# Kernel tuning notes

Measured on AMD Instinct MI355X. Metric: run time of the kernel, lower is better.

## Reference

```python
import jax, jax.numpy as jnp
import numpy as np

T, B, E, H = 2048, 2, 1024, 16

def setup_inputs() -> dict:
    rng = jax.random.key(0)
    ks = jax.random.split(rng, 7)
    s = 0.02
    return {
        "query": jax.random.normal(ks[0], (T, B, E), jnp.float32),
        "key": jax.random.normal(ks[1], (T, B, E), jnp.float32),
        "value": jax.random.normal(ks[2], (T, B, E), jnp.float32),
        "in_proj_weight": jax.random.normal(ks[3], (3 * E, E), jnp.float32) * s,
        "in_proj_bias": jax.random.normal(ks[4], (3 * E,), jnp.float32) * s,
        "out_proj_weight": jax.random.normal(ks[5], (E, E), jnp.float32) * s,
        "out_proj_bias": jax.random.normal(ks[6], (E,), jnp.float32) * s,
    }

def reference(query, key, value, in_proj_weight, in_proj_bias, out_proj_weight, out_proj_bias):
    tgt_len, bsz, embed_dim = query.shape
    num_heads = H
    head_dim = embed_dim // num_heads
    scaling = head_dim ** -0.5
    wq, wk, wv = jnp.split(in_proj_weight, 3, axis=0)
    bq, bk, bv = jnp.split(in_proj_bias, 3, axis=0)
    # projections: F.linear(x, W, b) = x @ W.T + b
    q = (query @ wq.T + bq) * scaling          # (T, B, E)
    k = key @ wk.T + bk                        # (S, B, E)
    v = value @ wv.T + bv                      # (S, B, E)
    # (len, B, E) -> (B*H, len, head_dim), matching torch view+transpose
    def to_heads(x):
        L = x.shape[0]
        return x.reshape(L, bsz * num_heads, head_dim).transpose(1, 0, 2)
    q, k, v = to_heads(q), to_heads(k), to_heads(v)
    scores = jnp.einsum('bqd,bkd->bqk', q, k)  # (B*H, T, S)
    attn = jax.nn.softmax(scores, axis=-1)
    out = jnp.einsum('bqk,bkd->bqd', attn, v)  # (B*H, T, head_dim)
    out = out.transpose(1, 0, 2).reshape(tgt_len, bsz, embed_dim)
    out = out @ out_proj_weight.T + out_proj_bias
    return out
```

## Files before the change

### kernel.cpp

```cpp
#include <hip/hip_runtime.h>
#include <cstdint>
#include <cstddef>

#define QSCALE 0.18033688011112042f

typedef __attribute__((ext_vector_type(8))) short bf16x8;
typedef __attribute__((ext_vector_type(4))) float f32x4;

#define MFMA(a, b, c) __builtin_amdgcn_mfma_f32_16x16x32_bf16(a, b, c, 0, 0, 0)

typedef union { unsigned int u[4]; bf16x8 b; } pku;

__device__ __forceinline__ unsigned short cvt_bf16(float x) {
  union { float f; unsigned int u; } v;
  v.f = x;
  unsigned int r = v.u + 0x7FFFu + ((v.u >> 16) & 1u);
  return (unsigned short)(r >> 16);
}

__device__ __forceinline__ void gll16(const void* g, void* l) {
  __builtin_amdgcn_global_load_lds(
      (const __attribute__((address_space(1))) unsigned int*)g,
      (__attribute__((address_space(3))) unsigned int*)l, 16, 0, 0);
}

__device__ __forceinline__ float fast_exp2(float x) {
#if __has_builtin(__builtin_amdgcn_exp2f)
  return __builtin_amdgcn_exp2f(x);
#else
  float r; asm("v_exp_f32 %0, %1" : "=v"(r) : "v"(x)); return r;
#endif
}

__device__ __forceinline__ unsigned int pack_bf16(float lo, float hi) {
  union { float f; unsigned int u; } a, b;
  a.f = lo; b.f = hi;
  return __builtin_amdgcn_perm(b.u + 0x8000u, a.u + 0x8000u, 0x07060302u);
}

__global__ void cvt_all(const float* __restrict__ q,
                        const float* __restrict__ k,
                        const float* __restrict__ v,
                        const float* __restrict__ ipw,
                        const float* __restrict__ opw,
                        unsigned short* __restrict__ dst) {
  const size_t i = ((size_t)blockIdx.x * 256 + threadIdx.x) * 8;
  const float* src;
  float scale = 1.0f;
  if (i < 4194304) src = q + i;
  else if (i < 8388608) src = k + (i - 4194304);
  else if (i < 12582912) src = v + (i - 8388608);
  else {
    const size_t w = i - 12582912;
    if (w < 3145728) { src = ipw + w; if (w < 1048576) scale = QSCALE; }
    else src = opw + (w - 3145728);
  }
  float4 a = *(const float4*)src;
  float4 b = *(const float4*)(src + 4);
  uint4 o;
  o.x = cvt_bf16(a.x * scale) | ((unsigned int)cvt_bf16(a.y * scale) << 16);
  o.y = cvt_bf16(a.z * scale) | ((unsigned int)cvt_bf16(a.w * scale) << 16);
  o.z = cvt_bf16(b.x * scale) | ((unsigned int)cvt_bf16(b.y * scale) << 16);
  o.w = cvt_bf16(b.z * scale) | ((unsigned int)cvt_bf16(b.w * scale) << 16);
  *(uint4*)(dst + i) = o;
}

__global__ __launch_bounds__(256, 3) void gemm_qkv(
    const unsigned short* __restrict__ X,
    const unsigned short* __restrict__ W,
    const float* __restrict__ bias,
    unsigned short* __restrict__ Qh,
    unsigned short* __restrict__ Kh,
    unsigned short* __restrict__ Vt)
{
  __shared__ unsigned short As[128 * 64];
  __shared__ unsigned short Bs[128 * 64];
  const int tid = threadIdx.x;
  const int wave = tid >> 6, lane = tid & 63;
  const int quad = lane >> 4, l16 = lane & 15;
  const int flat = blockIdx.x + (blockIdx.y << 3) + (blockIdx.z << 8);
  const int nf = (flat & 7) * 96 + (flat >> 3);
  const int z = nf >> 8;
  const int m0 = ((nf >> 3) & 31) * 128;
  const int n0 = (nf & 7) * 128;
  const unsigned short* Ab = X + (size_t)z * 4194304 + (size_t)m0 * 1024;
  const unsigned short* Bb = W + ((size_t)z * 1024 + n0) * 1024;
  const int wr = (wave >> 1) * 64, wc = (wave & 1) * 64;

  const f32x4 z4 = {0.f, 0.f, 0.f, 0.f};
  f32x4 acc[4][4];
#pragma unroll
  for (int i = 0; i < 4; ++i)
#pragma unroll
    for (int j = 0; j < 4; ++j) acc[i][j] = z4;

  for (int k0 = 0; k0 < 1024; k0 += 64) {
    __syncthreads();
#pragma unroll
    for (int j = 0; j < 4; ++j) {
      const int c = j * 256 + tid;
      const int row = c >> 3, pc = c & 7;
      const int kc = pc ^ (row & 7);
      gll16(Ab + (size_t)row * 1024 + k0 + kc * 8, &As[c * 8]);
      gll16(Bb + (size_t)row * 1024 + k0 + kc * 8, &Bs[c * 8]);
    }
    __syncthreads();
#pragma unroll
    for (int kk = 0; kk < 2; ++kk) {
      bf16x8 af[4], bfr[4];
#pragma unroll
      for (int rt = 0; rt < 4; ++rt) {
        const int row = wr + rt * 16 + l16;
        af[rt] = *(const bf16x8*)&As[row * 64 + ((kk * 4 + quad) ^ (row & 7)) * 8];
      }
#pragma unroll
      for (int ct = 0; ct < 4; ++ct) {
        const int row = wc + ct * 16 + l16;
        bfr[ct] = *(const bf16x8*)&Bs[row * 64 + ((kk * 4 + quad) ^ (row & 7)) * 8];
      }
#pragma unroll
      for (int rt = 0; rt < 4; ++rt)
#pragma unroll
        for (int ct = 0; ct < 4; ++ct)
          acc[rt][ct] = MFMA(af[rt], bfr[ct], acc[rt][ct]);
    }
  }

#pragma unroll
  for (int rt = 0; rt < 4; ++rt)
#pragma unroll
    for (int ct = 0; ct < 4; ++ct) {
      const int gn = n0 + wc + ct * 16 + l16;
      float bv = bias[z * 1024 + gn];
      if (z == 0) bv *= QSCALE;
      const int h = gn >> 6, d = gn & 63;
#pragma unroll
      for (int r = 0; r < 4; ++r) {
        const int gm = m0 + wr + rt * 16 + quad * 4 + r;
        const int t = gm >> 1, b = gm & 1;
        const int bh = b * 16 + h;
        const unsigned short o = cvt_bf16(acc[rt][ct][r] + bv);
        if (z == 0)      Qh[((size_t)bh * 2048 + t) * 64 + d] = o;
        else if (z == 1) Kh[((size_t)bh * 2048 + t) * 64 + d] = o;
        else {
          const int w32 = t & 31;
          const int tp = (t & ~31) | (((w32 >> 2) & 3) << 3) | ((w32 >> 4) << 2) | (w32 & 3);
          Vt[((size_t)bh * 64 + d) * 2048 + tp] = o;
        }
      }
    }
}

__global__ __launch_bounds__(256, 2) void attn(
    const unsigned short* __restrict__ Qh,
    const unsigned short* __restrict__ Kh,
    const unsigned short* __restrict__ Vt,
    unsigned short* __restrict__ O)
{
  __shared__ unsigned short KV[2][16384];
  __shared__ float Ls[128];
  const int tid = threadIdx.x;
  const int wave = tid >> 6, lane = tid & 63;
  const int quad = lane >> 4, l16 = lane & 15;
  const int pair = wave >> 1, kh = wave & 1;
  const int flat = blockIdx.x + (blockIdx.y << 4);
  const int nf = (flat & 7) * 64 + (flat >> 3);
  const int qt = nf & 15, bh = nf >> 4;
  const unsigned short* Qb = Qh + ((size_t)bh * 2048 + qt * 128 + pair * 64) * 64;
  const unsigned short* Kb = Kh + (size_t)bh * 2048 * 64;
  const unsigned short* Vb = Vt + (size_t)bh * 64 * 2048;

  bf16x8 qf[4][2];
#pragma unroll
  for (int g = 0; g < 4; ++g)
#pragma unroll
    for (int kk = 0; kk < 2; ++kk)
      qf[g][kk] = *(const bf16x8*)(Qb + (size_t)(g * 16 + l16) * 64 + kk * 32 + quad * 8);

  const unsigned short* kp[4];
  const unsigned short* vp[4];
  int klo[4], vlo[4];
#pragma unroll
  for (int j = 0; j < 4; ++j) {
    const int c = wave * 256 + j * 64 + lane;
    const int r = c >> 3, cc = c & 7;
    kp[j] = Kb + (size_t)r * 64 + (cc ^ (r & 7)) * 8;
    klo[j] = c * 8;
    const int r2 = c >> 4, cc2 = c & 15;
    vp[j] = Vb + (size_t)r2 * 2048 + (cc2 ^ (r2 & 15)) * 8;
    vlo[j] = 8192 + c * 8;
  }

  pku ones;
  ones.u[0] = ones.u[1] = ones.u[2] = ones.u[3] = 0x3F803F80u;

  const f32x4 z4 = {0.f, 0.f, 0.f, 0.f};
  f32x4 oacc[4][4];
  f32x4 lacc[4] = {z4, z4, z4, z4};
#pragma unroll
  for (int g = 0; g < 4; ++g)
#pragma unroll
    for (int c = 0; c < 4; ++c) oacc[g][c] = z4;

#pragma unroll
  for (int j = 0; j < 4; ++j) {
    gll16(kp[j], &KV[0][klo[j]]);
    gll16(vp[j], &KV[0][vlo[j]]);
    kp[j] += 128 * 64;
    vp[j] += 128;
  }
  __syncthreads();

#pragma unroll 1
  for (int it = 0; it < 16; ++it) {
    const int cur = it & 1;
    if (it < 15) {
#pragma unroll
      for (int j = 0; j < 4; ++j) {
        gll16(kp[j], &KV[cur ^ 1][klo[j]]);
        gll16(vp[j], &KV[cur ^ 1][vlo[j]]);
        kp[j] += 128 * 64;
        vp[j] += 128;
      }
    }
    const unsigned short* Ks = KV[cur];
    const unsigned short* Vs = KV[cur] + 8192;

#pragma unroll
    for (int jj = 0; jj < 2; ++jj) {
      unsigned int pk0[4][2], pk1[4][2];
#pragma unroll
      for (int half = 0; half < 2; ++half) {
        const int ct = jj * 2 + half;
        const int R = kh * 64 + ct * 16 + l16;
        bf16x8 kfr[2];
#pragma unroll
        for (int kk = 0; kk < 2; ++kk)
          kfr[kk] = *(const bf16x8*)&Ks[R * 64 + ((kk * 4 + quad) ^ (R & 7)) * 8];
#pragma unroll
        for (int g = 0; g < 4; ++g) {
          f32x4 sv = z4;
          sv = MFMA(kfr[0], qf[g][0], sv);
          sv = MFMA(kfr[1], qf[g][1], sv);
          f32x4 p;
#pragma unroll
          for (int r = 0; r < 4; ++r) p[r] = fast_exp2(sv[r]);
          pk0[g][half] = pack_bf16(p[0], p[1]);
          pk1[g][half] = pack_bf16(p[2], p[3]);
        }
      }
      const int jjg = kh * 2 + jj;
#pragma unroll
      for (int ctd = 0; ctd < 4; ++ctd) {
        const int R = ctd * 16 + l16;
        const int phys = (jjg * 4 + quad) ^ (R & 15);
        const bf16x8 vv = *(const bf16x8*)&Vs[R * 128 + phys * 8];
#pragma unroll
        for (int g = 0; g < 4; ++g) {
          pku a;
          a.u[0] = pk0[g][0]; a.u[1] = pk1[g][0];
          a.u[2] = pk0[g][1]; a.u[3] = pk1[g][1];
          oacc[g][ctd] = MFMA(a.b, vv, oacc[g][ctd]);
        }
      }
#pragma unroll
      for (int g = 0; g < 4; ++g) {
        pku a;
        a.u[0] = pk0[g][0]; a.u[1] = pk1[g][0];
        a.u[2] = pk0[g][1]; a.u[3] = pk1[g][1];
        lacc[g] = MFMA(a.b, ones.b, lacc[g]);
      }
    }
    __syncthreads();
  }

  float* Fp = (float*)KV;
  if (kh == 1) {
#pragma unroll
    for (int g = 0; g < 4; ++g) {
#pragma unroll
      for (int ctd = 0; ctd < 4; ++ctd)
#pragma unroll
        for (int r = 0; r < 4; ++r)
          Fp[pair * 4096 + (g * 16 + quad * 4 + r) * 64 + ctd * 16 + l16] = oacc[g][ctd][r];
#pragma unroll
      for (int r = 0; r < 4; ++r)
        Ls[pair * 64 + g * 16 + quad * 4 + r] = lacc[g][r];
    }
  }
  __syncthreads();
  if (kh == 0) {
    const int b = bh >> 4, h = bh & 15;
#pragma unroll
    for (int g = 0; g < 4; ++g)
#pragma unroll
      for (int r = 0; r < 4; ++r) {
        const int ql = g * 16 + quad * 4 + r;
        const float lv = lacc[g][r] + Ls[pair * 64 + ql];
        const float inv = 1.0f / lv;
        const int t = qt * 128 + pair * 64 + ql;
#pragma unroll
        for (int ctd = 0; ctd < 4; ++ctd) {
          const float val = oacc[g][ctd][r] + Fp[pair * 4096 + ql * 64 + ctd * 16 + l16];
          O[((size_t)t * 2 + b) * 1024 + h * 64 + ctd * 16 + l16] = cvt_bf16(val * inv);
        }
      }
  }
}

__global__ __launch_bounds__(256, 2) void gemm_out(
    const unsigned short* __restrict__ A,
    const unsigned short* __restrict__ W,
    const float* __restrict__ bias,
    float* __restrict__ out)
{
  __shared__ unsigned short As[2][128 * 64];
  __shared__ unsigned short Bs[2][64 * 64];
  const int tid = threadIdx.x;
  const int wave = tid >> 6, lane = tid & 63;
  const int quad = lane >> 4, l16 = lane & 15;
  const int flat = blockIdx.x + (blockIdx.y << 4);
  const int nf = (flat & 7) * 64 + (flat >> 3);
  const int m0 = (nf >> 4) * 128;
  const int n0 = (nf & 15) * 64;
  const unsigned short* Ab = A + (size_t)m0 * 1024;
  const unsigned short* Bb = W + (size_t)n0 * 1024;
  const int wr = (wave >> 1) * 64, wc = (wave & 1) * 32;

  auto stage = [&](int k0, int buf) {
#pragma unroll
    for (int j = 0; j < 4; ++j) {
      const int c = j * 256 + tid;
      const int row = c >> 3, pc = c & 7;
      const int kc = pc ^ (row & 7);
      gll16(Ab + (size_t)row * 1024 + k0 + kc * 8, &As[buf][c * 8]);
    }
#pragma unroll
    for (int j = 0; j < 2; ++j) {
      const int c = j * 256 + tid;
      const int row = c >> 3, pc = c & 7;
      const int kc = pc ^ (row & 7);
      gll16(Bb + (size_t)row * 1024 + k0 + kc * 8, &Bs[buf][c * 8]);
    }
  };

  const f32x4 z4 = {0.f, 0.f, 0.f, 0.f};
  f32x4 acc[4][2];
#pragma unroll
  for (int i = 0; i < 4; ++i)
#pragma unroll
    for (int j = 0; j < 2; ++j) acc[i][j] = z4;

  stage(0, 0);
  __syncthreads();

  for (int k0 = 0; k0 < 1024; k0 += 64) {
    const int cur = (k0 >> 6) & 1;
    if (k0 < 960) stage(k0 + 64, cur ^ 1);
#pragma unroll
    for (int kk = 0; kk < 2; ++kk) {
      bf16x8 af[4], bfr[2];
#pragma unroll
      for (int rt = 0; rt < 4; ++rt) {
        const int row = wr + rt * 16 + l16;
        af[rt] = *(const bf16x8*)&As[cur][row * 64 + ((kk * 4 + quad) ^ (row & 7)) * 8];
      }
#pragma unroll
      for (int ct = 0; ct < 2; ++ct) {
        const int row = wc + ct * 16 + l16;
        bfr[ct] = *(const bf16x8*)&Bs[cur][row * 64 + ((kk * 4 + quad) ^ (row & 7)) * 8];
      }
#pragma unroll
      for (int rt = 0; rt < 4; ++rt)
#pragma unroll
        for (int ct = 0; ct < 2; ++ct)
          acc[rt][ct] = MFMA(af[rt], bfr[ct], acc[rt][ct]);
    }
    __syncthreads();
  }

#pragma unroll
  for (int rt = 0; rt < 4; ++rt)
#pragma unroll
    for (int ct = 0; ct < 2; ++ct) {
      const int gn = n0 + wc + ct * 16 + l16;
      const float bv = bias[gn];
#pragma unroll
      for (int r = 0; r < 4; ++r) {
        const int gm = m0 + wr + rt * 16 + quad * 4 + r;
        out[(size_t)gm * 1024 + gn] = acc[rt][ct][r] + bv;
      }
    }
}

extern "C" void kernel_launch(void* const* d_in, const int* in_sizes, int n_in,
                              void* d_out, int out_size, void* d_ws, size_t ws_size,
                              hipStream_t stream) {
  const float* q   = (const float*)d_in[0];
  const float* k   = (const float*)d_in[1];
  const float* v   = (const float*)d_in[2];
  const float* ipw = (const float*)d_in[3];
  const float* ipb = (const float*)d_in[4];
  const float* opw = (const float*)d_in[5];
  const float* opb = (const float*)d_in[6];

  unsigned short* ws = (unsigned short*)d_ws;
  unsigned short* X  = ws;
  unsigned short* Wb = ws + 12582912;
  unsigned short* Wo = ws + 15728640;
  unsigned short* Qh = ws + 16777216;
  unsigned short* Kh = ws + 20971520;
  unsigned short* Vx = ws + 25165824;
  unsigned short* Oa = ws + 29360128;

  cvt_all<<<dim3(8192), 256, 0, stream>>>(q, k, v, ipw, opw, ws);
  gemm_qkv<<<dim3(8, 32, 3), 256, 0, stream>>>(X, Wb, ipb, Qh, Kh, Vx);
  attn<<<dim3(16, 32), 256, 0, stream>>>(Qh, Kh, Vx, Oa);
  gemm_out<<<dim3(16, 32), 256, 0, stream>>>(Oa, Wo, opb, (float*)d_out);
}
```

Before: 211.2 us.

## Double-buffer QKV GEMM and use single explicit waitcnt barrier per pipeline step

The QKV projection GEMM moves from a single shared buffer with two barriers per k-step to a double-buffered pipeline, prefetching the next k-tile while the current one runs on MFMA. Its occupancy hint drops from 3 to 2 blocks per CU to make room for the larger shared buffer. All three kernels (QKV GEMM, attention, out-proj GEMM) replace their end-of-iteration __syncthreads with one PIPE_SYNC at the top of each step: an explicit vmcnt(0) wait plus s_barrier fenced by sched_barriers. The goal is to overlap global-to-LDS loads with compute and cut barrier count, at the cost of lower occupancy in the QKV GEMM.

```diff
diff --git a/kernel.cpp b/kernel.cpp
--- a/kernel.cpp
+++ b/kernel.cpp
@@ -8,6 +8,13 @@
 typedef __attribute__((ext_vector_type(4))) float f32x4;
 
 #define MFMA(a, b, c) __builtin_amdgcn_mfma_f32_16x16x32_bf16(a, b, c, 0, 0, 0)
+
+#define PIPE_SYNC() do {                                   \
+    asm volatile("s_waitcnt vmcnt(0)" ::: "memory");       \
+    __builtin_amdgcn_sched_barrier(0);                     \
+    __builtin_amdgcn_s_barrier();                          \
+    __builtin_amdgcn_sched_barrier(0);                     \
+  } while (0)
 
 typedef union { unsigned int u[4]; bf16x8 b; } pku;
 
@@ -65,7 +72,7 @@
   *(uint4*)(dst + i) = o;
 }
 
-__global__ __launch_bounds__(256, 3) void gemm_qkv(
+__global__ __launch_bounds__(256, 2) void gemm_qkv(
     const unsigned short* __restrict__ X,
     const unsigned short* __restrict__ W,
     const float* __restrict__ bias,
@@ -73,8 +80,7 @@
     unsigned short* __restrict__ Kh,
     unsigned short* __restrict__ Vt)
 {
-  __shared__ unsigned short As[128 * 64];
-  __shared__ unsigned short Bs[128 * 64];
+  __shared__ unsigned short S[2][16384];
   const int tid = threadIdx.x;
   const int wave = tid >> 6, lane = tid & 63;
   const int quad = lane >> 4, l16 = lane & 15;
@@ -94,17 +100,26 @@
 #pragma unroll
     for (int j = 0; j < 4; ++j) acc[i][j] = z4;
 
-  for (int k0 = 0; k0 < 1024; k0 += 64) {
-    __syncthreads();
+  auto stage = [&](int k0, int buf) {
 #pragma unroll
     for (int j = 0; j < 4; ++j) {
       const int c = j * 256 + tid;
       const int row = c >> 3, pc = c & 7;
       const int kc = pc ^ (row & 7);
-      gll16(Ab + (size_t)row * 1024 + k0 + kc * 8, &As[c * 8]);
-      gll16(Bb + (size_t)row * 1024 + k0 + kc * 8, &Bs[c * 8]);
-    }
-    __syncthreads();
+      gll16(Ab + (size_t)row * 1024 + k0 + kc * 8, &S[buf][c * 8]);
+      gll16(Bb + (size_t)row * 1024 + k0 + kc * 8, &S[buf][8192 + c * 8]);
+    }
+  };
+
+  stage(0, 0);
+
+#pragma unroll 1
+  for (int t = 0; t < 16; ++t) {
+    const int cur = t & 1;
+    PIPE_SYNC();
+    if (t < 15) stage((t + 1) * 64, cur ^ 1);
+    const unsigned short* As = S[cur];
+    const unsigned short* Bs = S[cur] + 8192;
 #pragma unroll
     for (int kk = 0; kk < 2; ++kk) {
       bf16x8 af[4], bfr[4];
@@ -209,11 +224,11 @@
     kp[j] += 128 * 64;
     vp[j] += 128;
   }
-  __syncthreads();
 
 #pragma unroll 1
   for (int it = 0; it < 16; ++it) {
     const int cur = it & 1;
+    PIPE_SYNC();
     if (it < 15) {
 #pragma unroll
       for (int j = 0; j < 4; ++j) {
@@ -271,9 +286,9 @@
         lacc[g] = MFMA(a.b, ones.b, lacc[g]);
       }
     }
-    __syncthreads();
-  }
-
+  }
+
+  __syncthreads();
   float* Fp = (float*)KV;
   if (kh == 1) {
 #pragma unroll
@@ -352,10 +367,11 @@
     for (int j = 0; j < 2; ++j) acc[i][j] = z4;
 
   stage(0, 0);
-  __syncthreads();
-
+
+#pragma unroll 1
   for (int k0 = 0; k0 < 1024; k0 += 64) {
     const int cur = (k0 >> 6) & 1;
+    PIPE_SYNC();
     if (k0 < 960) stage(k0 + 64, cur ^ 1);
 #pragma unroll
     for (int kk = 0; kk < 2; ++kk) {
@@ -376,7 +392,6 @@
         for (int ct = 0; ct < 2; ++ct)
           acc[rt][ct] = MFMA(af[rt], bfr[ct], acc[rt][ct]);
     }
-    __syncthreads();
   }
 
 #pragma unroll
```

Result: no change. 211.4 us (+0.1%).

## Fuse fp32-to-bf16 conversion into GEMM loads and tighten attention pipeline sync

Applied to the files above, without the earlier changes.

Drops the separate conversion kernel. The QKV and output GEMMs now read fp32 inputs and weights directly and convert to bf16 while writing to LDS, which removes one launch and a full bf16 round trip through global memory. The attention loop moves its barrier to the top of each iteration with an explicit vmcnt wait and raises wave priority around the PV MFMAs. The cost is that the GEMMs lose async global-to-LDS loads: gemm_out drops to single buffering with higher occupancy, and each GEMM block re-converts the weights it reads instead of using a precomputed bf16 copy.

```diff
diff --git a/kernel.cpp b/kernel.cpp
--- a/kernel.cpp
+++ b/kernel.cpp
@@ -8,6 +8,13 @@
 typedef __attribute__((ext_vector_type(4))) float f32x4;
 
 #define MFMA(a, b, c) __builtin_amdgcn_mfma_f32_16x16x32_bf16(a, b, c, 0, 0, 0)
+
+#define PIPE_SYNC() do {                                   \
+    asm volatile("s_waitcnt vmcnt(0)" ::: "memory");       \
+    __builtin_amdgcn_sched_barrier(0);                     \
+    __builtin_amdgcn_s_barrier();                          \
+    __builtin_amdgcn_sched_barrier(0);                     \
+  } while (0)
 
 typedef union { unsigned int u[4]; bf16x8 b; } pku;
 
@@ -38,36 +45,20 @@
   return __builtin_amdgcn_perm(b.u + 0x8000u, a.u + 0x8000u, 0x07060302u);
 }
 
-__global__ void cvt_all(const float* __restrict__ q,
-                        const float* __restrict__ k,
-                        const float* __restrict__ v,
-                        const float* __restrict__ ipw,
-                        const float* __restrict__ opw,
-                        unsigned short* __restrict__ dst) {
-  const size_t i = ((size_t)blockIdx.x * 256 + threadIdx.x) * 8;
-  const float* src;
-  float scale = 1.0f;
-  if (i < 4194304) src = q + i;
-  else if (i < 8388608) src = k + (i - 4194304);
-  else if (i < 12582912) src = v + (i - 8388608);
-  else {
-    const size_t w = i - 12582912;
-    if (w < 3145728) { src = ipw + w; if (w < 1048576) scale = QSCALE; }
-    else src = opw + (w - 3145728);
-  }
-  float4 a = *(const float4*)src;
-  float4 b = *(const float4*)(src + 4);
+__device__ __forceinline__ uint4 cvt8(float4 a, float4 b, float sc) {
   uint4 o;
-  o.x = cvt_bf16(a.x * scale) | ((unsigned int)cvt_bf16(a.y * scale) << 16);
-  o.y = cvt_bf16(a.z * scale) | ((unsigned int)cvt_bf16(a.w * scale) << 16);
-  o.z = cvt_bf16(b.x * scale) | ((unsigned int)cvt_bf16(b.y * scale) << 16);
-  o.w = cvt_bf16(b.z * scale) | ((unsigned int)cvt_bf16(b.w * scale) << 16);
-  *(uint4*)(dst + i) = o;
+  o.x = pack_bf16(a.x * sc, a.y * sc);
+  o.y = pack_bf16(a.z * sc, a.w * sc);
+  o.z = pack_bf16(b.x * sc, b.y * sc);
+  o.w = pack_bf16(b.z * sc, b.w * sc);
+  return o;
 }
 
 __global__ __launch_bounds__(256, 3) void gemm_qkv(
-    const unsigned short* __restrict__ X,
-    const unsigned short* __restrict__ W,
+    const float* __restrict__ Qf,
+    const float* __restrict__ Kf,
+    const float* __restrict__ Vf,
+    const float* __restrict__ Wf,
     const float* __restrict__ bias,
     unsigned short* __restrict__ Qh,
     unsigned short* __restrict__ Kh,
@@ -83,8 +74,9 @@
   const int z = nf >> 8;
   const int m0 = ((nf >> 3) & 31) * 128;
   const int n0 = (nf & 7) * 128;
-  const unsigned short* Ab = X + (size_t)z * 4194304 + (size_t)m0 * 1024;
-  const unsigned short* Bb = W + ((size_t)z * 1024 + n0) * 1024;
+  const float* Ab = (z == 0 ? Qf : (z == 1 ? Kf : Vf)) + (size_t)m0 * 1024;
+  const float* Bb = Wf + ((size_t)z * 1024 + n0) * 1024;
+  const float wsc = (z == 0) ? QSCALE : 1.0f;
   const int wr = (wave >> 1) * 64, wc = (wave & 1) * 64;
 
   const f32x4 z4 = {0.f, 0.f, 0.f, 0.f};
@@ -100,9 +92,15 @@
     for (int j = 0; j < 4; ++j) {
       const int c = j * 256 + tid;
       const int row = c >> 3, pc = c & 7;
-      const int kc = pc ^ (row & 7);
-      gll16(Ab + (size_t)row * 1024 + k0 + kc * 8, &As[c * 8]);
-      gll16(Bb + (size_t)row * 1024 + k0 + kc * 8, &Bs[c * 8]);
+      const int swz = (pc ^ (row & 7)) * 8;
+      const float* sa = Ab + (size_t)row * 1024 + k0 + pc * 8;
+      const float4 a0 = *(const float4*)sa;
+      const float4 a1 = *(const float4*)(sa + 4);
+      *(uint4*)&As[row * 64 + swz] = cvt8(a0, a1, 1.0f);
+      const float* sb = Bb + (size_t)row * 1024 + k0 + pc * 8;
+      const float4 b0 = *(const float4*)sb;
+      const float4 b1 = *(const float4*)(sb + 4);
+      *(uint4*)&Bs[row * 64 + swz] = cvt8(b0, b1, wsc);
     }
     __syncthreads();
 #pragma unroll
@@ -209,11 +207,11 @@
     kp[j] += 128 * 64;
     vp[j] += 128;
   }
-  __syncthreads();
 
 #pragma unroll 1
   for (int it = 0; it < 16; ++it) {
     const int cur = it & 1;
+    PIPE_SYNC();
     if (it < 15) {
 #pragma unroll
       for (int j = 0; j < 4; ++j) {
@@ -250,6 +248,7 @@
         }
       }
       const int jjg = kh * 2 + jj;
+      __builtin_amdgcn_s_setprio(1);
 #pragma unroll
       for (int ctd = 0; ctd < 4; ++ctd) {
         const int R = ctd * 16 + l16;
@@ -270,10 +269,11 @@
         a.u[2] = pk0[g][1]; a.u[3] = pk1[g][1];
         lacc[g] = MFMA(a.b, ones.b, lacc[g]);
       }
-    }
-    __syncthreads();
-  }
-
+      __builtin_amdgcn_s_setprio(0);
+    }
+  }
+
+  __syncthreads();
   float* Fp = (float*)KV;
   if (kh == 1) {
 #pragma unroll
@@ -308,14 +308,14 @@
   }
 }
 
-__global__ __launch_bounds__(256, 2) void gemm_out(
+__global__ __launch_bounds__(256, 4) void gemm_out(
     const unsigned short* __restrict__ A,
-    const unsigned short* __restrict__ W,
+    const float* __restrict__ Wf,
     const float* __restrict__ bias,
     float* __restrict__ out)
 {
-  __shared__ unsigned short As[2][128 * 64];
-  __shared__ unsigned short Bs[2][64 * 64];
+  __shared__ unsigned short As[128 * 64];
+  __shared__ unsigned short Bs[64 * 64];
   const int tid = threadIdx.x;
   const int wave = tid >> 6, lane = tid & 63;
   const int quad = lane >> 4, l16 = lane & 15;
@@ -324,51 +324,47 @@
   const int m0 = (nf >> 4) * 128;
   const int n0 = (nf & 15) * 64;
   const unsigned short* Ab = A + (size_t)m0 * 1024;
-  const unsigned short* Bb = W + (size_t)n0 * 1024;
+  const float* Bb = Wf + (size_t)n0 * 1024;
   const int wr = (wave >> 1) * 64, wc = (wave & 1) * 32;
 
-  auto stage = [&](int k0, int buf) {
+  const f32x4 z4 = {0.f, 0.f, 0.f, 0.f};
+  f32x4 acc[4][2];
+#pragma unroll
+  for (int i = 0; i < 4; ++i)
+#pragma unroll
+    for (int j = 0; j < 2; ++j) acc[i][j] = z4;
+
+  for (int k0 = 0; k0 < 1024; k0 += 64) {
+    __syncthreads();
 #pragma unroll
     for (int j = 0; j < 4; ++j) {
       const int c = j * 256 + tid;
       const int row = c >> 3, pc = c & 7;
       const int kc = pc ^ (row & 7);
-      gll16(Ab + (size_t)row * 1024 + k0 + kc * 8, &As[buf][c * 8]);
+      gll16(Ab + (size_t)row * 1024 + k0 + kc * 8, &As[c * 8]);
     }
 #pragma unroll
     for (int j = 0; j < 2; ++j) {
       const int c = j * 256 + tid;
       const int row = c >> 3, pc = c & 7;
-      const int kc = pc ^ (row & 7);
-      gll16(Bb + (size_t)row * 1024 + k0 + kc * 8, &Bs[buf][c * 8]);
-    }
-  };
-
-  const f32x4 z4 = {0.f, 0.f, 0.f, 0.f};
-  f32x4 acc[4][2];
-#pragma unroll
-  for (int i = 0; i < 4; ++i)
-#pragma unroll
-    for (int j = 0; j < 2; ++j) acc[i][j] = z4;
-
-  stage(0, 0);
-  __syncthreads();
-
-  for (int k0 = 0; k0 < 1024; k0 += 64) {
-    const int cur = (k0 >> 6) & 1;
-    if (k0 < 960) stage(k0 + 64, cur ^ 1);
+      const float* sb = Bb + (size_t)row * 1024 + k0 + pc * 8;
+      const float4 b0 = *(const float4*)sb;
+      const float4 b1 = *(const float4*)(sb + 4);
+      *(uint4*)&Bs[row * 64 + (pc ^ (row & 7)) * 8] = cvt8(b0, b1, 1.0f);
+    }
+    __syncthreads();
 #pragma unroll
     for (int kk = 0; kk < 2; ++kk) {
       bf16x8 af[4], bfr[2];
 #pragma unroll
       for (int rt = 0; rt < 4; ++rt) {
         const int row = wr + rt * 16 + l16;
-        af[rt] = *(const bf16x8*)&As[cur][row * 64 + ((kk * 4 + quad) ^ (row & 7)) * 8];
+        af[rt] = *(const bf16x8*)&As[row * 64 + ((kk * 4 + quad) ^ (row & 7)) * 8];
       }
 #pragma unroll
       for (int ct = 0; ct < 2; ++ct) {
         const int row = wc + ct * 16 + l16;
-        bfr[ct] = *(const bf16x8*)&Bs[cur][row * 64 + ((kk * 4 + quad) ^ (row & 7)) * 8];
+        bfr[ct] = *(const bf16x8*)&Bs[row * 64 + ((kk * 4 + quad) ^ (row & 7)) * 8];
       }
 #pragma unroll
       for (int rt = 0; rt < 4; ++rt)
@@ -376,7 +372,6 @@
         for (int ct = 0; ct < 2; ++ct)
           acc[rt][ct] = MFMA(af[rt], bfr[ct], acc[rt][ct]);
     }
-    __syncthreads();
   }
 
 #pragma unroll
@@ -405,16 +400,12 @@
   const float* opb = (const float*)d_in[6];
 
   unsigned short* ws = (unsigned short*)d_ws;
-  unsigned short* X  = ws;
-  unsigned short* Wb = ws + 12582912;
-  unsigned short* Wo = ws + 15728640;
-  unsigned short* Qh = ws + 16777216;
-  unsigned short* Kh = ws + 20971520;
-  unsigned short* Vx = ws + 25165824;
-  unsigned short* Oa = ws + 29360128;
-
-  cvt_all<<<dim3(8192), 256, 0, stream>>>(q, k, v, ipw, opw, ws);
-  gemm_qkv<<<dim3(8, 32, 3), 256, 0, stream>>>(X, Wb, ipb, Qh, Kh, Vx);
+  unsigned short* Qh = ws;
+  unsigned short* Kh = ws + 4194304;
+  unsigned short* Vx = ws + 8388608;
+  unsigned short* Oa = ws + 12582912;
+
+  gemm_qkv<<<dim3(8, 32, 3), 256, 0, stream>>>(q, k, v, ipw, ipb, Qh, Kh, Vx);
   attn<<<dim3(16, 32), 256, 0, stream>>>(Qh, Kh, Vx, Oa);
-  gemm_out<<<dim3(16, 32), 256, 0, stream>>>(Oa, Wo, opb, (float*)d_out);
-}
+  gemm_out<<<dim3(16, 32), 256, 0, stream>>>(Oa, opw, opb, (float*)d_out);
+}
```

After: 225.9 us. +6.9%, slower.
